# Kernel tuning notes

Hardware: AMD Instinct MI355X
Metric: run time of the kernel (lower is better)

## Reference

```python
import jax, jax.numpy as jnp
import numpy as np

EPS_BN = 1e-5
EPS_W = 1e-8


def setup_inputs() -> dict:
    key = jax.random.key(0)
    ks = jax.random.split(key, 6)
    B, N, S, D1, D2 = 8, 8192, 2048, 128, 256
    Cin = D1 + D2  # 384
    return {
        "points_position": jax.random.normal(ks[0], (B, 3, N), jnp.float32),
        "sampled_points_position": jax.random.normal(ks[1], (B, 3, S), jnp.float32),
        "skip_points_feature": jax.random.normal(ks[2], (B, D1, N), jnp.float32),
        "sampled_points_feature": jax.random.normal(ks[3], (B, D2, S), jnp.float32),
        "W1": jax.random.normal(ks[4], (256, Cin), jnp.float32) * 0.05,
        "b1": jnp.zeros((256,), jnp.float32),
        "g1": jnp.ones((256,), jnp.float32),
        "beta1": jnp.zeros((256,), jnp.float32),
        "W2": jax.random.normal(ks[5], (128, 256), jnp.float32) * 0.05,
        "b2": jnp.zeros((128,), jnp.float32),
        "g2": jnp.ones((128,), jnp.float32),
        "beta2": jnp.zeros((128,), jnp.float32),
    }


def _bn_relu(x, g, b):
    # train-mode BatchNorm1d over (batch, points) per channel, x: [B,N,C]
    mean = jnp.mean(x, axis=(0, 1), keepdims=True)
    var = jnp.mean(jnp.square(x - mean), axis=(0, 1), keepdims=True)  # biased var
    return jax.nn.relu((x - mean) * jax.lax.rsqrt(var + EPS_BN) * g + b)


def reference(points_position, sampled_points_position, skip_points_feature,
              sampled_points_feature, W1, b1, g1, beta1, W2, b2, g2, beta2):
    pos = points_position.transpose(0, 2, 1)            # [B,N,3]
    spos = sampled_points_position.transpose(0, 2, 1)   # [B,S,3]
    sfeat = sampled_points_feature.transpose(0, 2, 1)   # [B,S,D2]

    # squared pairwise distance [B,N,S]
    d = (jnp.sum(pos * pos, axis=-1, keepdims=True)
         - 2.0 * jnp.einsum("bnc,bsc->bns", pos, spos)
         + jnp.sum(spos * spos, axis=-1)[:, None, :])

    # 3 nearest neighbors (smallest distances)
    neg_d3, idx = jax.lax.top_k(-d, 3)                  # [B,N,3]
    d3 = -neg_d3
    w = 1.0 / (d3 + EPS_W)
    w = w / jnp.sum(w, axis=-1, keepdims=True)          # [B,N,3]

    gathered = jax.vmap(lambda f, i: f[i])(sfeat, idx)  # [B,N,3,D2]
    interp = jnp.einsum("bnk,bnkd->bnd", w, gathered)   # [B,N,D2]

    feat = jnp.concatenate([skip_points_feature.transpose(0, 2, 1), interp], axis=-1)  # [B,N,D1+D2]

    h = _bn_relu(jnp.einsum("bnc,oc->bno", feat, W1) + b1, g1, beta1)  # [B,N,256]
    h = _bn_relu(jnp.einsum("bnc,oc->bno", h, W2) + b2, g2, beta2)     # [B,N,128]
    return h.transpose(0, 2, 1)                          # [B,128,N]
```

## Files before the change

### kernel.cpp

```cpp
#include <hip/hip_runtime.h>

constexpr int BATCH = 8;
constexpr int NPT   = 8192;
constexpr int NSMP  = 2048;
constexpr int D1C   = 128;
constexpr int D2C   = 256;
constexpr int CIN   = 384;
constexpr int C1    = 256;
constexpr int C2    = 128;
constexpr int BN_TOTAL = BATCH * NPT;

constexpr int BM = 128, BK = 32;
constexpr int NRB = BN_TOTAL / BM;
constexpr int NRW = NRB * 2;

typedef __bf16 bf16x8 __attribute__((ext_vector_type(8)));
typedef short  s16x8  __attribute__((ext_vector_type(8)));
typedef float  f32x4  __attribute__((ext_vector_type(4)));

__device__ __forceinline__ unsigned short f2bf(float x) {
  unsigned u = __builtin_bit_cast(unsigned, x);
  u += 0x7fffu + ((u >> 16) & 1u);
  return (unsigned short)(u >> 16);
}
__device__ __forceinline__ float bf2f(unsigned short h) {
  return __builtin_bit_cast(float, (unsigned)h << 16);
}

__device__ __forceinline__ void gld_lds16(const void* g, void* l) {
  __builtin_amdgcn_global_load_lds(
      (const __attribute__((address_space(1))) void*)g,
      (__attribute__((address_space(3))) void*)l, 16, 0, 0);
}

__global__ void transpose_k(const float* __restrict__ in, float* __restrict__ out,
                            int rows, int cols, long inBatch, long outBatch) {
  __shared__ float tile[32][33];
  const float* inb = in + (size_t)blockIdx.z * inBatch;
  float* outb = out + (size_t)blockIdx.z * outBatch;
  int c0 = blockIdx.x * 32;
  int r0 = blockIdx.y * 32;
  int tx = threadIdx.x, ty = threadIdx.y;
#pragma unroll
  for (int i = 0; i < 32; i += 8) {
    int r = r0 + ty + i;
    tile[ty + i][tx] = inb[(size_t)r * cols + c0 + tx];
  }
  __syncthreads();
#pragma unroll
  for (int i = 0; i < 32; i += 8) {
    int c = c0 + ty + i;
    outb[(size_t)c * rows + r0 + tx] = tile[tx][ty + i];
  }
}

__global__ void skip_to_featB(const float* __restrict__ skip,
                              unsigned short* __restrict__ featB) {
  __shared__ float tile[32][33];
  int b = blockIdx.z;
  int n0 = blockIdx.x * 32;
  int d0 = blockIdx.y * 32;
  int tx = threadIdx.x, ty = threadIdx.y;
#pragma unroll
  for (int i = 0; i < 32; i += 8) {
    tile[ty + i][tx] = skip[((size_t)b * D1C + d0 + ty + i) * NPT + n0 + tx];
  }
  __syncthreads();
#pragma unroll
  for (int i = 0; i < 32; i += 8) {
    int n = n0 + ty + i;
    featB[((size_t)b * NPT + n) * CIN + d0 + tx] = f2bf(tile[tx][ty + i]);
  }
}

__global__ void wprep_both(const float* __restrict__ W1, unsigned short* __restrict__ W1h,
                           const float* __restrict__ W2, unsigned short* __restrict__ W2h) {
  int i = blockIdx.x * 256 + threadIdx.x;
  if (i < C1 * CIN) W1h[i] = f2bf(W1[i]);
  if (i < C2 * C1)  W2h[i] = f2bf(W2[i]);
}

__global__ void pack_spos(const float* __restrict__ spos, float* __restrict__ sposI,
                          float4* __restrict__ qs4) {
  int g = blockIdx.x * 256 + threadIdx.x;
  int b = g >> 11, s = g & (NSMP - 1);
  const float* sp = spos + (size_t)b * 3 * NSMP;
  float x = sp[s], y = sp[NSMP + s], z = sp[2 * NSMP + s];
  sposI[(size_t)g * 3 + 0] = x;
  sposI[(size_t)g * 3 + 1] = y;
  sposI[(size_t)g * 3 + 2] = z;
  qs4[g] = make_float4(-2.f * x, -2.f * y, -2.f * z,
                       fmaf(x, x, fmaf(y, y, z * z)));
}

constexpr int SEG = NSMP / 4;

__device__ __forceinline__ void ins_med3(float kf, float& k0, float& k1,
                                         float& k2, float& k3) {
  float o0 = k0, o1 = k1, o2 = k2;
  k0 = fminf(kf, o0);
  k1 = __builtin_amdgcn_fmed3f(kf, o0, o1);
  k2 = __builtin_amdgcn_fmed3f(kf, o1, o2);
  k3 = __builtin_amdgcn_fmed3f(kf, o2, k3);
}

__global__ __launch_bounds__(256) void knn_kernel(
    const float* __restrict__ pos,
    const float4* __restrict__ qs4g,
    const float* __restrict__ sposI,
    int* __restrict__ idx_out,
    float* __restrict__ wgt_out,
    int* __restrict__ flag_list,
    int* __restrict__ flag_count) {
  __shared__ float mk[4][4][64];

  int tid = threadIdx.x;
  int wave = tid >> 6, lane = tid & 63;
  int blk = blockIdx.x;
  int b = blk >> 7;
  int n = ((blk & 127) << 6) + lane;

  const float* pb = pos + (size_t)b * 3 * NPT;
  float px = pb[n], py = pb[NPT + n], pz = pb[2 * NPT + n];
  float pp = fmaf(px, px, fmaf(py, py, pz * pz));

  const float INF = __builtin_inff();
  float k0 = INF, k1 = INF, k2 = INF, k3 = INF;

  int s0 = wave * SEG;
  const float4* qseg = qs4g + (size_t)b * NSMP + __builtin_amdgcn_readfirstlane(s0);

#define KNN_STEP(Q, SS)                                                   \
  {                                                                       \
    float d_ = fmaf(px, (Q).x, fmaf(py, (Q).y, fmaf(pz, (Q).z, (Q).w + pp))); \
    unsigned ki_ = (__builtin_bit_cast(unsigned, d_) & 0xFFFFF800u) |     \
                   (unsigned)(SS);                                        \
    ins_med3(__builtin_bit_cast(float, ki_), k0, k1, k2, k3);             \
  }

  for (int t = 0; t < SEG; t += 8) {
    float4 qv[8];
#pragma unroll
    for (int u = 0; u < 8; u++) qv[u] = qseg[t + u];
#pragma unroll
    for (int u = 0; u < 8; u++) KNN_STEP(qv[u], s0 + t + u)
  }
#undef KNN_STEP

  mk[wave][0][lane] = k0; mk[wave][1][lane] = k1;
  mk[wave][2][lane] = k2; mk[wave][3][lane] = k3;
  __syncthreads();

  if (tid < 64) {
    float K0 = INF, K1 = INF, K2 = INF, K3 = INF;
#pragma unroll
    for (int w = 0; w < 4; w++)
#pragma unroll
      for (int sl = 0; sl < 4; sl++)
        ins_med3(mk[w][sl][tid], K0, K1, K2, K3);

    int p = blk * 64 + tid;
    int I0 = (int)(__builtin_bit_cast(unsigned, K0) & 0x7FFu);
    int I1 = (int)(__builtin_bit_cast(unsigned, K1) & 0x7FFu);
    int I2 = (int)(__builtin_bit_cast(unsigned, K2) & 0x7FFu);
    float d2m = __builtin_bit_cast(float, __builtin_bit_cast(unsigned, K2) & 0xFFFFF800u);
    float d3m = __builtin_bit_cast(float, __builtin_bit_cast(unsigned, K3) & 0xFFFFF800u);
    bool flag = (d3m - d2m) < 2e-3f * fmaxf(d3m, 0.f) + 1e-5f;
    if (flag) {
      int slot = atomicAdd(flag_count, 1);
      flag_list[slot] = p;
    }
    const float* q = sposI + (size_t)b * 3 * NSMP;
    double pxd = (double)px, pyd = (double)py, pzd = (double)pz;
    double dd[3]; int II[3] = {I0, I1, I2};
#pragma unroll
    for (int k = 0; k < 3; k++) {
      double dx = pxd - (double)q[3 * II[k]];
      double dy = pyd - (double)q[3 * II[k] + 1];
      double dz = pzd - (double)q[3 * II[k] + 2];
      dd[k] = dx * dx + dy * dy + dz * dz;
    }
    double w0 = 1.0 / (dd[0] + 1e-8);
    double w1 = 1.0 / (dd[1] + 1e-8);
    double w2 = 1.0 / (dd[2] + 1e-8);
    double inv = 1.0 / (w0 + w1 + w2);
    size_t o = (size_t)p * 3;
    idx_out[o + 0] = I0; idx_out[o + 1] = I1; idx_out[o + 2] = I2;
    wgt_out[o + 0] = (float)(w0 * inv);
    wgt_out[o + 1] = (float)(w1 * inv);
    wgt_out[o + 2] = (float)(w2 * inv);
  }
}

__device__ __forceinline__ bool dless(double d, int i, double D, int I) {
  return d < D || (d == D && i < I);
}
__device__ __forceinline__ void dins3(double d, int i,
                                      double& b0, double& b1, double& b2,
                                      int& i0, int& i1, int& i2) {
  if (dless(d, i, b2, i2)) {
    if (dless(d, i, b1, i1)) {
      b2 = b1; i2 = i1;
      if (dless(d, i, b0, i0)) { b1 = b0; i1 = i0; b0 = d; i0 = i; }
      else                     { b1 = d; i1 = i; }
    } else { b2 = d; i2 = i; }
  }
}

__global__ __launch_bounds__(256) void knn_fallback(
    const float* __restrict__ pos, const float* __restrict__ sposI,
    const int* __restrict__ flag_list, const int* __restrict__ flag_count,
    int* __restrict__ idx_out, float* __restrict__ wgt_out) {
  int wave = threadIdx.x >> 6, lane = threadIdx.x & 63;
  int gw = blockIdx.x * 4 + wave;
  int cnt = *flag_count;
  for (int t = gw; t < cnt; t += 1024) {
    int p = flag_list[t];
    int b = p >> 13, n = p & (NPT - 1);
    const float* pb = pos + (size_t)b * 3 * NPT;
    double px = (double)pb[n], py = (double)pb[NPT + n], pz = (double)pb[2 * NPT + n];
    const float* q = sposI + (size_t)b * 3 * NSMP;
    double b0 = 1e300, b1 = 1e300, b2 = 1e300;
    int i0 = 0x7FFFFFFF, i1 = 0x7FFFFFFF, i2 = 0x7FFFFFFF;
    for (int s = lane; s < NSMP; s += 64) {
      double dx = px - (double)q[3 * s];
      double dy = py - (double)q[3 * s + 1];
      double dz = pz - (double)q[3 * s + 2];
      double d = dx * dx + dy * dy + dz * dz;
      dins3(d, s, b0, b1, b2, i0, i1, i2);
    }
#pragma unroll
    for (int m = 1; m < 64; m <<= 1) {
      double o0 = __shfl_xor(b0, m, 64), o1 = __shfl_xor(b1, m, 64), o2 = __shfl_xor(b2, m, 64);
      int    j0 = __shfl_xor(i0, m, 64), j1 = __shfl_xor(i1, m, 64), j2 = __shfl_xor(i2, m, 64);
      dins3(o0, j0, b0, b1, b2, i0, i1, i2);
      dins3(o1, j1, b0, b1, b2, i0, i1, i2);
      dins3(o2, j2, b0, b1, b2, i0, i1, i2);
    }
    if (lane == 0) {
      double w0 = 1.0 / (b0 + 1e-8);
      double w1 = 1.0 / (b1 + 1e-8);
      double w2 = 1.0 / (b2 + 1e-8);
      double inv = 1.0 / (w0 + w1 + w2);
      size_t o = (size_t)p * 3;
      idx_out[o + 0] = i0; idx_out[o + 1] = i1; idx_out[o + 2] = i2;
      wgt_out[o + 0] = (float)(w0 * inv);
      wgt_out[o + 1] = (float)(w1 * inv);
      wgt_out[o + 2] = (float)(w2 * inv);
    }
  }
}

constexpr int IPB = 16;
__global__ __launch_bounds__(256) void interp_kernel(
    const float* __restrict__ sfeatT,
    const int* __restrict__ idx,
    const float* __restrict__ wgt,
    unsigned short* __restrict__ featB) {
  int c = threadIdx.x;
  int p0 = blockIdx.x * IPB;
  int b = p0 >> 13;
  const float* base = sfeatT + (size_t)b * NSMP * D2C;
#pragma unroll 4
  for (int pi = 0; pi < IPB; pi++) {
    int p = p0 + pi;
    size_t o = (size_t)p * 3;
    int i0 = idx[o], i1 = idx[o + 1], i2 = idx[o + 2];
    float w0 = wgt[o], w1 = wgt[o + 1], w2 = wgt[o + 2];
    float v = w0 * base[(size_t)i0 * D2C + c]
            + w1 * base[(size_t)i1 * D2C + c]
            + w2 * base[(size_t)i2 * D2C + c];
    featB[(size_t)p * CIN + D1C + c] = f2bf(v);
  }
}

__global__ __launch_bounds__(256) void gemm1_mw(
    const unsigned short* __restrict__ featB,
    const unsigned short* __restrict__ W1h,
    const float* __restrict__ bias,
    unsigned short* __restrict__ Y1,
    float* __restrict__ part_s,
    float* __restrict__ part_q) {
  __shared__ __align__(16) unsigned short As[BM * BK];
  __shared__ __align__(16) unsigned short Bs[BM * BK];
  int tid = threadIdx.x;
  int lane = tid & 63, w = tid >> 6;
  int wr = w >> 1, wc = w & 1;
  int m16 = lane & 15, quad = lane >> 4;
  int cb = blockIdx.x, rb = blockIdx.y;
  int row0 = rb * BM, col0 = cb * BM;
  int srow = lane >> 2, scol8 = (lane & 3) * 8;

  f32x4 acc[4][4];
#pragma unroll
  for (int j = 0; j < 4; j++) {
    float bj = bias[col0 + wc * 64 + j * 16 + m16];
#pragma unroll
    for (int i = 0; i < 4; i++) acc[i][j] = f32x4{bj, bj, bj, bj};
  }

  for (int k0 = 0; k0 < CIN; k0 += BK) {
#pragma unroll
    for (int kq = 0; kq < 2; kq++) {
      int ar = 32 * w + 16 * kq + srow;
      int lb = __builtin_amdgcn_readfirstlane((32 * w + 16 * kq) * BK);
      gld_lds16(&featB[(size_t)(row0 + ar) * CIN + k0 + scol8], &As[lb]);
      gld_lds16(&W1h[(size_t)(col0 + ar) * CIN + k0 + scol8], &Bs[lb]);
    }
    __syncthreads();

    bf16x8 a[4], bb[4];
#pragma unroll
    for (int i = 0; i < 4; i++)
      a[i] = __builtin_bit_cast(bf16x8,
          *(const s16x8*)&As[(wr * 64 + i * 16 + m16) * BK + quad * 8]);
#pragma unroll
    for (int j = 0; j < 4; j++)
      bb[j] = __builtin_bit_cast(bf16x8,
          *(const s16x8*)&Bs[(wc * 64 + j * 16 + m16) * BK + quad * 8]);
#pragma unroll
    for (int i = 0; i < 4; i++)
#pragma unroll
      for (int j = 0; j < 4; j++)
        acc[i][j] = __builtin_amdgcn_mfma_f32_16x16x32_bf16(a[i], bb[j], acc[i][j], 0, 0, 0);
    __syncthreads();
  }

#pragma unroll
  for (int j = 0; j < 4; j++) {
    int col = col0 + wc * 64 + j * 16 + m16;
    float s = 0.f, q = 0.f;
#pragma unroll
    for (int i = 0; i < 4; i++)
#pragma unroll
      for (int r = 0; r < 4; r++) {
        float v = acc[i][j][r];
        Y1[(size_t)(row0 + wr * 64 + i * 16 + quad * 4 + r) * C1 + col] = f2bf(v);
        s += v; q = fmaf(v, v, q);
      }
    s += __shfl_xor(s, 16, 64); s += __shfl_xor(s, 32, 64);
    q += __shfl_xor(q, 16, 64); q += __shfl_xor(q, 32, 64);
    if (quad == 0) {
      part_s[(size_t)col * NRW + rb * 2 + wr] = s;
      part_q[(size_t)col * NRW + rb * 2 + wr] = q;
    }
  }
}

__global__ __launch_bounds__(256) void gemm2_mw(
    const unsigned short* __restrict__ Y1,
    const float* __restrict__ scale1, const float* __restrict__ shift1,
    const unsigned short* __restrict__ W2h,
    const float* __restrict__ bias,
    unsigned short* __restrict__ Y2,
    float* __restrict__ part_s,
    float* __restrict__ part_q) {
  __shared__ __align__(16) unsigned short As[BM * BK];
  __shared__ __align__(16) unsigned short Bs[BM * BK];
  __shared__ float scs[C1], shs[C1];
  int tid = threadIdx.x;
  int lane = tid & 63, w = tid >> 6;
  int wr = w >> 1, wc = w & 1;
  int m16 = lane & 15, quad = lane >> 4;
  int rb = blockIdx.x;
  int row0 = rb * BM, col0 = 0;
  int srow = lane >> 2, scol8 = (lane & 3) * 8;

  scs[tid] = scale1[tid]; shs[tid] = shift1[tid];

  f32x4 acc[4][4];
#pragma unroll
  for (int j = 0; j < 4; j++) {
    float bj = bias[col0 + wc * 64 + j * 16 + m16];
#pragma unroll
    for (int i = 0; i < 4; i++) acc[i][j] = f32x4{bj, bj, bj, bj};
  }
  __syncthreads();

  for (int k0 = 0; k0 < C1; k0 += BK) {
#pragma unroll
    for (int kq = 0; kq < 2; kq++) {
      int ar = 32 * w + 16 * kq + srow;
      int lb = __builtin_amdgcn_readfirstlane((32 * w + 16 * kq) * BK);
      gld_lds16(&W2h[(size_t)(col0 + ar) * C1 + k0 + scol8], &Bs[lb]);
      s16x8 v = *(const s16x8*)&Y1[(size_t)(row0 + ar) * C1 + k0 + scol8];
      unsigned short ov[8];
#pragma unroll
      for (int e = 0; e < 8; e++) {
        float x = bf2f((unsigned short)v[e]);
        float y = fmaxf(fmaf(x, scs[k0 + scol8 + e], shs[k0 + scol8 + e]), 0.f);
        ov[e] = f2bf(y);
      }
      *(s16x8*)&As[ar * BK + scol8] = *(const s16x8*)ov;
    }
    __syncthreads();

    bf16x8 a[4], bb[4];
#pragma unroll
    for (int i = 0; i < 4; i++)
      a[i] = __builtin_bit_cast(bf16x8,
          *(const s16x8*)&As[(wr * 64 + i * 16 + m16) * BK + quad * 8]);
#pragma unroll
    for (int j = 0; j < 4; j++)
      bb[j] = __builtin_bit_cast(bf16x8,
          *(const s16x8*)&Bs[(wc * 64 + j * 16 + m16) * BK + quad * 8]);
#pragma unroll
    for (int i = 0; i < 4; i++)
#pragma unroll
      for (int j = 0; j < 4; j++)
        acc[i][j] = __builtin_amdgcn_mfma_f32_16x16x32_bf16(a[i], bb[j], acc[i][j], 0, 0, 0);
    __syncthreads();
  }

#pragma unroll
  for (int j = 0; j < 4; j++) {
    int col = col0 + wc * 64 + j * 16 + m16;
    float s = 0.f, q = 0.f;
#pragma unroll
    for (int i = 0; i < 4; i++)
#pragma unroll
      for (int r = 0; r < 4; r++) {
        float v = acc[i][j][r];
        Y2[(size_t)(row0 + wr * 64 + i * 16 + quad * 4 + r) * C2 + col] = f2bf(v);
        s += v; q = fmaf(v, v, q);
      }
    s += __shfl_xor(s, 16, 64); s += __shfl_xor(s, 32, 64);
    q += __shfl_xor(q, 16, 64); q += __shfl_xor(q, 32, 64);
    if (quad == 0) {
      part_s[(size_t)col * NRW + rb * 2 + wr] = s;
      part_q[(size_t)col * NRW + rb * 2 + wr] = q;
    }
  }
}

__global__ __launch_bounds__(256) void bn_reduce_coef(
    const float* __restrict__ part_s, const float* __restrict__ part_q, int nrb,
    const float* __restrict__ g, const float* __restrict__ beta,
    float* __restrict__ scale, float* __restrict__ shift) {
  int ch = blockIdx.x;
  int tid = threadIdx.x;
  float s = 0.f, q = 0.f;
  for (int t = tid; t < nrb; t += 256) {
    s += part_s[(size_t)ch * nrb + t];
    q += part_q[(size_t)ch * nrb + t];
  }
#pragma unroll
  for (int m = 1; m < 64; m <<= 1) {
    s += __shfl_xor(s, m, 64);
    q += __shfl_xor(q, m, 64);
  }
  __shared__ float ls[4], lq[4];
  int wave = tid >> 6;
  if ((tid & 63) == 0) { ls[wave] = s; lq[wave] = q; }
  __syncthreads();
  if (tid == 0) {
    s = ls[0] + ls[1] + ls[2] + ls[3];
    q = lq[0] + lq[1] + lq[2] + lq[3];
    const float invBN = 1.0f / (float)BN_TOTAL;
    float mean = s * invBN;
    float var = q * invBN - mean * mean;
    float sc = g[ch] / sqrtf(var + 1e-5f);
    scale[ch] = sc;
    shift[ch] = beta[ch] - mean * sc;
  }
}

__global__ void final_kernel(const unsigned short* __restrict__ Y2,
                             const float* __restrict__ scale, const float* __restrict__ shift,
                             float* __restrict__ out) {
  __shared__ float tile[32][33];
  int b = blockIdx.z;
  int n0 = blockIdx.x * 32;
  int c0 = blockIdx.y * 32;
  int tx = threadIdx.x, ty = threadIdx.y;
  float sc = scale[c0 + tx];
  float sh = shift[c0 + tx];
#pragma unroll
  for (int i = 0; i < 32; i += 8) {
    int n = n0 + ty + i;
    float v = bf2f(Y2[((size_t)b * NPT + n) * C2 + c0 + tx]);
    tile[ty + i][tx] = fmaxf(fmaf(v, sc, sh), 0.f);
  }
  __syncthreads();
#pragma unroll
  for (int i = 0; i < 32; i += 8) {
    int c = c0 + ty + i;
    out[((size_t)b * C2 + c) * NPT + n0 + tx] = tile[tx][ty + i];
  }
}

extern "C" void kernel_launch(void* const* d_in, const int* in_sizes, int n_in,
                              void* d_out, int out_size, void* d_ws, size_t ws_size,
                              hipStream_t stream) {
  (void)in_sizes; (void)n_in; (void)out_size; (void)ws_size;
  const float* pos   = (const float*)d_in[0];
  const float* spos  = (const float*)d_in[1];
  const float* skip  = (const float*)d_in[2];
  const float* sfeat = (const float*)d_in[3];
  const float* W1    = (const float*)d_in[4];
  const float* b1    = (const float*)d_in[5];
  const float* g1    = (const float*)d_in[6];
  const float* beta1 = (const float*)d_in[7];
  const float* W2    = (const float*)d_in[8];
  const float* b2    = (const float*)d_in[9];
  const float* g2    = (const float*)d_in[10];
  const float* beta2 = (const float*)d_in[11];
  float* out = (float*)d_out;

  float* ws = (float*)d_ws;
  size_t off = 0;
  float* sfeatT  = ws + off; off += (size_t)BATCH * NSMP * D2C;
  unsigned short* featB = (unsigned short*)(ws + off); off += (size_t)BN_TOTAL * CIN / 2;
  unsigned short* Y1    = (unsigned short*)(ws + off); off += (size_t)BN_TOTAL * C1 / 2;
  unsigned short* Y2    = (unsigned short*)(ws + off); off += (size_t)BN_TOTAL * C2 / 2;
  unsigned short* W1h   = (unsigned short*)(ws + off); off += (size_t)C1 * CIN / 2;
  unsigned short* W2h   = (unsigned short*)(ws + off); off += (size_t)C2 * C1 / 2;
  int*   knn_idx = (int*)(ws + off); off += (size_t)BN_TOTAL * 3;
  float* knn_w   = ws + off; off += (size_t)BN_TOTAL * 3;
  float* sposI   = ws + off; off += (size_t)BATCH * NSMP * 3;
  float4* qs4    = (float4*)(ws + off); off += (size_t)BATCH * NSMP * 4;
  int* flag_list = (int*)(ws + off); off += (size_t)BN_TOTAL;
  float* part1_s = ws + off; off += (size_t)C1 * NRW;
  float* part1_q = ws + off; off += (size_t)C1 * NRW;
  float* part2_s = ws + off; off += (size_t)C2 * NRW;
  float* part2_q = ws + off; off += (size_t)C2 * NRW;
  float* stats   = ws + off; off += 2048;
  int*   flag_count = (int*)stats;
  float* scale1 = stats + 256, *shift1 = stats + 512;
  float* scale2 = stats + 768, *shift2 = stats + 1024;

  hipMemsetAsync(flag_count, 0, sizeof(int), stream);

  dim3 tb(32, 8);
  transpose_k<<<dim3(NSMP / 32, D2C / 32, BATCH), tb, 0, stream>>>(
      sfeat, sfeatT, D2C, NSMP, (long)D2C * NSMP, (long)NSMP * D2C);
  wprep_both<<<(C1 * CIN + 255) / 256, 256, 0, stream>>>(W1, W1h, W2, W2h);
  skip_to_featB<<<dim3(NPT / 32, D1C / 32, BATCH), tb, 0, stream>>>(skip, featB);

  pack_spos<<<BATCH * NSMP / 256, 256, 0, stream>>>(spos, sposI, qs4);
  knn_kernel<<<BN_TOTAL / 64, 256, 0, stream>>>(pos, qs4, sposI, knn_idx, knn_w,
                                                flag_list, flag_count);
  knn_fallback<<<256, 256, 0, stream>>>(pos, sposI, flag_list, flag_count,
                                        knn_idx, knn_w);
  interp_kernel<<<BN_TOTAL / IPB, 256, 0, stream>>>(sfeatT, knn_idx, knn_w, featB);

  gemm1_mw<<<dim3(C1 / BM, NRB), 256, 0, stream>>>(
      featB, W1h, b1, Y1, part1_s, part1_q);
  bn_reduce_coef<<<C1, 256, 0, stream>>>(part1_s, part1_q, NRW, g1, beta1, scale1, shift1);

  gemm2_mw<<<NRB, 256, 0, stream>>>(
      Y1, scale1, shift1, W2h, b2, Y2, part2_s, part2_q);
  bn_reduce_coef<<<C2, 256, 0, stream>>>(part2_s, part2_q, NRW, g2, beta2, scale2, shift2);

  final_kernel<<<dim3(NPT / 32, C2 / 32, BATCH), tb, 0, stream>>>(Y2, scale2, shift2, out);
}
```

Measured before the change: 288.3 us.

## Merge prep kernels, split KNN scan over eight waves, drop per-point offset

```diff
diff --git a/kernel.cpp b/kernel.cpp
--- a/kernel.cpp
+++ b/kernel.cpp
@@ -73,27 +73,29 @@
   }
 }
 
-__global__ void wprep_both(const float* __restrict__ W1, unsigned short* __restrict__ W1h,
-                           const float* __restrict__ W2, unsigned short* __restrict__ W2h) {
-  int i = blockIdx.x * 256 + threadIdx.x;
-  if (i < C1 * CIN) W1h[i] = f2bf(W1[i]);
-  if (i < C2 * C1)  W2h[i] = f2bf(W2[i]);
-}
-
-__global__ void pack_spos(const float* __restrict__ spos, float* __restrict__ sposI,
-                          float4* __restrict__ qs4) {
+__global__ __launch_bounds__(256) void prep_misc(
+    const float* __restrict__ spos, float* __restrict__ sposI, float4* __restrict__ qs4,
+    const float* __restrict__ W1, unsigned short* __restrict__ W1h,
+    const float* __restrict__ W2, unsigned short* __restrict__ W2h,
+    int* __restrict__ flag_count) {
   int g = blockIdx.x * 256 + threadIdx.x;
-  int b = g >> 11, s = g & (NSMP - 1);
-  const float* sp = spos + (size_t)b * 3 * NSMP;
-  float x = sp[s], y = sp[NSMP + s], z = sp[2 * NSMP + s];
-  sposI[(size_t)g * 3 + 0] = x;
-  sposI[(size_t)g * 3 + 1] = y;
-  sposI[(size_t)g * 3 + 2] = z;
-  qs4[g] = make_float4(-2.f * x, -2.f * y, -2.f * z,
-                       fmaf(x, x, fmaf(y, y, z * z)));
-}
-
-constexpr int SEG = NSMP / 4;
+  if (g == 0) *flag_count = 0;
+  if (g < C1 * CIN) W1h[g] = f2bf(W1[g]);
+  if (g < C2 * C1)  W2h[g] = f2bf(W2[g]);
+  if (g < BATCH * NSMP) {
+    int b = g >> 11, s = g & (NSMP - 1);
+    const float* sp = spos + (size_t)b * 3 * NSMP;
+    float x = sp[s], y = sp[NSMP + s], z = sp[2 * NSMP + s];
+    sposI[(size_t)g * 3 + 0] = x;
+    sposI[(size_t)g * 3 + 1] = y;
+    sposI[(size_t)g * 3 + 2] = z;
+    qs4[g] = make_float4(-2.f * x, -2.f * y, -2.f * z,
+                         fmaf(x, x, fmaf(y, y, z * z)));
+  }
+}
+
+constexpr int KWAVES = 8;
+constexpr int SEGK = NSMP / KWAVES;
 
 __device__ __forceinline__ void ins_med3(float kf, float& k0, float& k1,
                                          float& k2, float& k3) {
@@ -104,7 +106,7 @@
   k3 = __builtin_amdgcn_fmed3f(kf, o2, k3);
 }
 
-__global__ __launch_bounds__(256) void knn_kernel(
+__global__ __launch_bounds__(512, 4) void knn_kernel(
     const float* __restrict__ pos,
     const float4* __restrict__ qs4g,
     const float* __restrict__ sposI,
@@ -112,7 +114,7 @@
     float* __restrict__ wgt_out,
     int* __restrict__ flag_list,
     int* __restrict__ flag_count) {
-  __shared__ float mk[4][4][64];
+  __shared__ float mk[KWAVES][4][64];
 
   int tid = threadIdx.x;
   int wave = tid >> 6, lane = tid & 63;
@@ -127,25 +129,23 @@
   const float INF = __builtin_inff();
   float k0 = INF, k1 = INF, k2 = INF, k3 = INF;
 
-  int s0 = wave * SEG;
-  const float4* qseg = qs4g + (size_t)b * NSMP + __builtin_amdgcn_readfirstlane(s0);
-
-#define KNN_STEP(Q, SS)                                                   \
-  {                                                                       \
-    float d_ = fmaf(px, (Q).x, fmaf(py, (Q).y, fmaf(pz, (Q).z, (Q).w + pp))); \
-    unsigned ki_ = (__builtin_bit_cast(unsigned, d_) & 0xFFFFF800u) |     \
-                   (unsigned)(SS);                                        \
-    ins_med3(__builtin_bit_cast(float, ki_), k0, k1, k2, k3);             \
-  }
-
-  for (int t = 0; t < SEG; t += 8) {
+  int s0 = wave * SEGK;
+  int tv = 0;
+  asm volatile("" : "+v"(tv));
+  const float4* qseg = qs4g + (size_t)b * NSMP + s0 + tv;
+
+  for (int t = 0; t < SEGK; t += 8) {
     float4 qv[8];
 #pragma unroll
     for (int u = 0; u < 8; u++) qv[u] = qseg[t + u];
 #pragma unroll
-    for (int u = 0; u < 8; u++) KNN_STEP(qv[u], s0 + t + u)
-  }
-#undef KNN_STEP
+    for (int u = 0; u < 8; u++) {
+      float d_ = fmaf(px, qv[u].x, fmaf(py, qv[u].y, fmaf(pz, qv[u].z, qv[u].w)));
+      unsigned ki_ = (__builtin_bit_cast(unsigned, d_) & 0xFFFFF800u) |
+                     (unsigned)(s0 + t + u);
+      ins_med3(__builtin_bit_cast(float, ki_), k0, k1, k2, k3);
+    }
+  }
 
   mk[wave][0][lane] = k0; mk[wave][1][lane] = k1;
   mk[wave][2][lane] = k2; mk[wave][3][lane] = k3;
@@ -154,7 +154,7 @@
   if (tid < 64) {
     float K0 = INF, K1 = INF, K2 = INF, K3 = INF;
 #pragma unroll
-    for (int w = 0; w < 4; w++)
+    for (int w = 0; w < KWAVES; w++)
 #pragma unroll
       for (int sl = 0; sl < 4; sl++)
         ins_med3(mk[w][sl][tid], K0, K1, K2, K3);
@@ -165,7 +165,7 @@
     int I2 = (int)(__builtin_bit_cast(unsigned, K2) & 0x7FFu);
     float d2m = __builtin_bit_cast(float, __builtin_bit_cast(unsigned, K2) & 0xFFFFF800u);
     float d3m = __builtin_bit_cast(float, __builtin_bit_cast(unsigned, K3) & 0xFFFFF800u);
-    bool flag = (d3m - d2m) < 2e-3f * fmaxf(d3m, 0.f) + 1e-5f;
+    bool flag = (d3m - d2m) < 2e-3f * (fabsf(d3m) + pp) + 1e-5f;
     if (flag) {
       int slot = atomicAdd(flag_count, 1);
       flag_list[slot] = p;
@@ -529,16 +529,14 @@
   float* scale1 = stats + 256, *shift1 = stats + 512;
   float* scale2 = stats + 768, *shift2 = stats + 1024;
 
-  hipMemsetAsync(flag_count, 0, sizeof(int), stream);
-
   dim3 tb(32, 8);
+  prep_misc<<<(C1 * CIN + 255) / 256, 256, 0, stream>>>(
+      spos, sposI, qs4, W1, W1h, W2, W2h, flag_count);
   transpose_k<<<dim3(NSMP / 32, D2C / 32, BATCH), tb, 0, stream>>>(
       sfeat, sfeatT, D2C, NSMP, (long)D2C * NSMP, (long)NSMP * D2C);
-  wprep_both<<<(C1 * CIN + 255) / 256, 256, 0, stream>>>(W1, W1h, W2, W2h);
   skip_to_featB<<<dim3(NPT / 32, D1C / 32, BATCH), tb, 0, stream>>>(skip, featB);
 
-  pack_spos<<<BATCH * NSMP / 256, 256, 0, stream>>>(spos, sposI, qs4);
-  knn_kernel<<<BN_TOTAL / 64, 256, 0, stream>>>(pos, qs4, sposI, knn_idx, knn_w,
+  knn_kernel<<<BN_TOTAL / 64, 512, 0, stream>>>(pos, qs4, sposI, knn_idx, knn_w,
                                                 flag_list, flag_count);
   knn_fallback<<<256, 256, 0, stream>>>(pos, sposI, flag_list, flag_count,
                                         knn_idx, knn_w);
```

Result: slower. 842.1 us (+192.1%).
